# Kernel tuning notes

Measured on AMD Instinct MI355X. Metric: run time of the kernel, lower is better.

The kernel has to match this reference:

```python
import jax, jax.numpy as jnp
import numpy as np
import math

L, D, H = 4, 256, 8
HD = D // H
B, SQ, SK = 2, 1024, 1024
FF = 3 * D
EPS = 1e-5


def setup_inputs() -> dict:
    key = jax.random.key(0)
    ks = jax.random.split(key, 16)
    s = 0.02
    w = lambda k, shape: jax.random.normal(k, shape, jnp.float32) * s
    return {
        "pose": jax.random.normal(ks[0], (B, SQ, D), jnp.float32),
        "vel": jax.random.normal(ks[1], (B, SK, D), jnp.float32),
        "img": jax.random.normal(ks[2], (B, SK, D), jnp.float32),
        "Wq": w(ks[3], (L, D, D)), "bq": jnp.zeros((L, D), jnp.float32),
        "Wk": w(ks[4], (L, D, D)), "bk": jnp.zeros((L, D), jnp.float32),
        "Wv": w(ks[5], (L, D, D)), "bv": jnp.zeros((L, D), jnp.float32),
        "Wo": w(ks[6], (L, D, D)), "bo": jnp.zeros((L, D), jnp.float32),
        "an_g": jnp.ones((L, D), jnp.float32), "an_b": jnp.zeros((L, D), jnp.float32),
        "W1": w(ks[7], (L, D, FF)), "b1": jnp.zeros((L, FF), jnp.float32),
        "W2": w(ks[8], (L, FF, D)), "b2": jnp.zeros((L, D), jnp.float32),
        "fn_g": jnp.ones((L, D), jnp.float32), "fn_b": jnp.zeros((L, D), jnp.float32),
        "n_g": jnp.ones((L, D), jnp.float32), "n_b": jnp.zeros((L, D), jnp.float32),
    }


def entmax15(x):
    # exact alpha=1.5 entmax along the last axis (Peters & Martins 2019)
    x = x * 0.5
    x = x - jnp.max(x, axis=-1, keepdims=True)
    z = -jnp.sort(-x, axis=-1)  # descending
    k = jnp.arange(1, z.shape[-1] + 1, dtype=x.dtype)
    mean = jnp.cumsum(z, axis=-1) / k
    mean_sq = jnp.cumsum(z * z, axis=-1) / k
    ss = k * (mean_sq - mean * mean)
    delta = jnp.clip((1.0 - ss) / k, 0.0)
    tau = mean - jnp.sqrt(delta)
    support = jnp.sum(tau <= z, axis=-1, keepdims=True)  # support size >= 1
    tau_star = jnp.take_along_axis(tau, support - 1, axis=-1)
    p = jnp.clip(x - tau_star, 0.0)
    return p * p


def layer_norm(x, g, b):
    m = jnp.mean(x, axis=-1, keepdims=True)
    v = jnp.mean((x - m) ** 2, axis=-1, keepdims=True)
    return (x - m) * jax.lax.rsqrt(v + EPS) * g + b


def mish(x):
    return x * jnp.tanh(jax.nn.softplus(x))


def reference(pose, vel, img, Wq, bq, Wk, bk, Wv, bv, Wo, bo, an_g, an_b,
              W1, b1, W2, b2, fn_g, fn_b, n_g, n_b):
    def mha(q_in, kv, i):
        bs, sq, _ = q_in.shape
        sk = kv.shape[1]
        q = (q_in @ Wq[i] + bq[i]).reshape(bs, sq, H, HD)
        k = (kv @ Wk[i] + bk[i]).reshape(bs, sk, H, HD)
        v = (kv @ Wv[i] + bv[i]).reshape(bs, sk, H, HD)
        scores = jnp.einsum('bqhd,bkhd->bhqk', q, k) / math.sqrt(HD)
        attn = entmax15(scores)
        out = jnp.einsum('bhqk,bkhd->bqhd', attn, v).reshape(bs, sq, D)
        return out @ Wo[i] + bo[i]

    def cross_layer(x1, x2, i):
        y = layer_norm(mha(x1, x2, i), an_g[i], an_b[i])
        x1 = x1 + y
        y = layer_norm(x1, fn_g[i], fn_b[i])
        h = mish(y @ W1[i] + b1[i]) @ W2[i] + b2[i]
        return x1 + h

    def stack(x, kv):
        for i in range(L):  # small fixed layer loop (shared weights across both paths)
            mem = x
            x = cross_layer(x, kv, i)
            x = layer_norm(x, n_g[i], n_b[i])
            x = x + mem
        return x

    img_out = stack(pose, img)
    pose_out = stack(pose, vel)
    return (pose_out, img_out)
```

## Files before the change

### kernel.cpp

```cpp
#include <hip/hip_runtime.h>
#include <math.h>

#define NL   4
#define DIM  256
#define NH   8
#define HDIM 32
#define SQL  1024
#define SKL  1024
#define FFD  768
#define CB   4
#define ROWS (CB * SQL)

typedef __attribute__((ext_vector_type(8))) short bf16x8;
typedef __attribute__((ext_vector_type(4))) short bf16x4;
typedef __attribute__((ext_vector_type(4))) float f32x4;
typedef __attribute__((ext_vector_type(2))) float f32x2;


__device__ __forceinline__ short f2bf(float f) {
    union { float f; unsigned u; } v; v.f = f;
    unsigned u = v.u + 0x7fffu + ((v.u >> 16) & 1u);
    return (short)(u >> 16);
}

__device__ __forceinline__ float fast_mish(float x) {
    float u = __expf(fminf(x, 20.0f));
    float a = __builtin_fmaf(u, u, 2.0f * u);
    return x * a * __builtin_amdgcn_rcpf(a + 2.0f);
}

__device__ __forceinline__ f32x2 lo2(f32x4 v) { return __builtin_shufflevector(v, v, 0, 1); }
__device__ __forceinline__ f32x2 hi2(f32x4 v) { return __builtin_shufflevector(v, v, 2, 3); }


__global__ __launch_bounds__(256) void init_kernel(
        const float* __restrict__ pose, const float* __restrict__ vel,
        const float* __restrict__ img, float* __restrict__ X,
        short* __restrict__ Xb, short* __restrict__ KVb) {
    int idx = blockIdx.x * 256 + threadIdx.x;
    if (idx >= CB * SQL * DIM) return;
    int c = idx / (SQL * DIM);
    int rem = idx - c * (SQL * DIM);
    int b = c & 1;
    float pv = pose[b * SQL * DIM + rem];
    X[idx]  = pv;
    Xb[idx] = f2bf(pv);
    const float* kv = (c < 2) ? vel : img;
    KVb[idx] = f2bf(kv[b * SQL * DIM + rem]);
}


__global__ __launch_bounds__(256) void transpose_all(
        const float* __restrict__ Wq, const float* __restrict__ Wk,
        const float* __restrict__ Wv, const float* __restrict__ Wo,
        const float* __restrict__ W1, const float* __restrict__ W2,
        short* __restrict__ Wqt, short* __restrict__ Wkt,
        short* __restrict__ Wvt, short* __restrict__ Wot,
        short* __restrict__ W1t, short* __restrict__ W2t) {
    __shared__ float tile[64][65];
    int z = blockIdx.x;
    const float* src; short* dst; int K, N, tx, ty;
    if (z < 256) {
        int m = z >> 6, lyr = (z >> 4) & 3, r = z & 15;
        src = ((m == 0) ? Wq : (m == 1) ? Wk : (m == 2) ? Wv : Wo) + (size_t)lyr * DIM * DIM;
        dst = ((m == 0) ? Wqt : (m == 1) ? Wkt : (m == 2) ? Wvt : Wot) + (size_t)lyr * DIM * DIM;
        K = DIM; N = DIM; tx = r & 3; ty = r >> 2;
    } else if (z < 448) {
        int idx = z - 256, lyr = idx / 48, r = idx % 48;
        src = W1 + (size_t)lyr * DIM * FFD; dst = W1t + (size_t)lyr * DIM * FFD;
        K = DIM; N = FFD; tx = r % 12; ty = r / 12;
    } else {
        int idx = z - 448, lyr = idx / 48, r = idx % 48;
        src = W2 + (size_t)lyr * FFD * DIM; dst = W2t + (size_t)lyr * FFD * DIM;
        K = FFD; N = DIM; tx = r % 4; ty = r / 4;
    }
    int t = threadIdx.x;
    int n0 = tx * 64, k0 = ty * 64;
#pragma unroll
    for (int i = 0; i < 16; i++) {
        int idx = t + i * 256;
        int r = idx >> 6, c = idx & 63;
        tile[r][c] = src[(size_t)(k0 + r) * N + n0 + c];
    }
    __syncthreads();
#pragma unroll
    for (int i = 0; i < 16; i++) {
        int idx = t + i * 256;
        int r = idx >> 6, c = idx & 63;
        dst[(size_t)(n0 + r) * K + k0 + c] = f2bf(tile[c][r]);
    }
}


__global__ __launch_bounds__(256) void kv_gemm(
        const short* __restrict__ KVb, const short* __restrict__ Wkt,
        const short* __restrict__ Wvt, const float* __restrict__ bk,
        const float* __restrict__ bv, short* __restrict__ Kb4,
        short* __restrict__ Vt4) {
    int z = blockIdx.z, lyr = z >> 1, kv = z & 1;
    const short* Wt   = (kv ? Wvt : Wkt) + (size_t)lyr * DIM * DIM;
    const float* bias = (kv ? bv : bk) + (size_t)lyr * DIM;

    int t = threadIdx.x, l = t & 63, w = t >> 6;
    int lq = l & 15, lg = l >> 4;
    int bm = blockIdx.y * 64, bn = blockIdx.x * 64;

    const short* ap = KVb + (size_t)(bm + w * 16 + lq) * DIM + lg * 8;
    const short* wp = Wt + (size_t)(bn + lq) * DIM + lg * 8;

    f32x4 acc[4];
#pragma unroll
    for (int nt = 0; nt < 4; nt++) acc[nt] = (f32x4){0.f, 0.f, 0.f, 0.f};
#pragma unroll
    for (int k0 = 0; k0 < DIM; k0 += 32) {
        bf16x8 af = *(const bf16x8*)(ap + k0);
#pragma unroll
        for (int nt = 0; nt < 4; nt++) {
            bf16x8 bfr = *(const bf16x8*)(wp + (size_t)nt * 16 * DIM + k0);
            acc[nt] = __builtin_amdgcn_mfma_f32_16x16x32_bf16(af, bfr, acc[nt], 0, 0, 0);
        }
    }

    int ms = bm + w * 16 + lg * 4;
#pragma unroll
    for (int nt = 0; nt < 4; nt++) {
        int col = bn + nt * 16 + lq;
        float bv_ = bias[col];
        if (kv == 0) {
            short* out = Kb4 + (size_t)lyr * ROWS * DIM;
#pragma unroll
            for (int j = 0; j < 4; j++)
                out[(size_t)(ms + j) * DIM + col] = f2bf(acc[nt][j] + bv_);
        } else {
            int cc = ms >> 10, kl = ms & 1023;
            bf16x4 pk;
#pragma unroll
            for (int j = 0; j < 4; j++) pk[j] = f2bf(acc[nt][j] + bv_);
            *(bf16x4*)(Vt4 + (size_t)lyr * ROWS * DIM + ((size_t)(cc * DIM + col)) * SKL + kl) = pk;
        }
    }
}


__global__ __launch_bounds__(512) void fused_tail(
        const short* __restrict__ T1b, const short* __restrict__ Wot,
        const float* __restrict__ bo, const float* __restrict__ Xres,
        const float* __restrict__ ag, const float* __restrict__ ab,
        const float* __restrict__ fg, const float* __restrict__ fb,
        const short* __restrict__ W1t, const float* __restrict__ b1,
        const short* __restrict__ W2t, const float* __restrict__ b2,
        const float* __restrict__ g_, const float* __restrict__ b_,
        float* __restrict__ outf, short* __restrict__ outb) {
    __shared__ float gbuf[16][264];
    __shared__ __align__(16) short y_lds[16][280];
    __shared__ __align__(16) short g1[16][792];
    float (*xbuf)[264] = (float(*)[264])g1;

    int t = threadIdx.x, l = t & 63, w = t >> 6;
    int lq = l & 15, lg = l >> 4;
    int bm = blockIdx.x * 16;

    {
        const short* ap = T1b + (size_t)(bm + lq) * DIM + lg * 8;
        const short* wp = Wot + (size_t)(w * 32 + lq) * DIM + lg * 8;
        f32x4 acc[2];
        acc[0] = (f32x4){0.f, 0.f, 0.f, 0.f};
        acc[1] = (f32x4){0.f, 0.f, 0.f, 0.f};
#pragma unroll
        for (int k0 = 0; k0 < DIM; k0 += 32) {
            bf16x8 af = *(const bf16x8*)(ap + k0);
#pragma unroll
            for (int nt = 0; nt < 2; nt++) {
                bf16x8 bfr = *(const bf16x8*)(wp + (size_t)nt * 16 * DIM + k0);
                acc[nt] = __builtin_amdgcn_mfma_f32_16x16x32_bf16(af, bfr, acc[nt], 0, 0, 0);
            }
        }
#pragma unroll
        for (int nt = 0; nt < 2; nt++) {
            int col = w * 32 + nt * 16 + lq;
            float bv_ = bo[col];
#pragma unroll
            for (int j = 0; j < 4; j++) gbuf[lg * 4 + j][col] = acc[nt][j] + bv_;
        }
    }
    __syncthreads();

    {
        int g = t >> 5, u = t & 31;
        int row = bm + g;
        float s = 0.f, s2 = 0.f;
#pragma unroll
        for (int i = 0; i < 8; i++) {
            float v = gbuf[g][u + 32 * i];
            s += v; s2 += v * v;
        }
#pragma unroll
        for (int off = 1; off < 32; off <<= 1) { s += __shfl_xor(s, off); s2 += __shfl_xor(s2, off); }
        float m = s * (1.f / DIM);
        float rstd = rsqrtf(s2 * (1.f / DIM) - m * m + 1e-5f);

        float x1v[8];
        float sb = 0.f, sb2 = 0.f;
#pragma unroll
        for (int i = 0; i < 8; i++) {
            int col = u + 32 * i;
            float x1 = Xres[(size_t)row * DIM + col] + (gbuf[g][col] - m) * rstd * ag[col] + ab[col];
            x1v[i] = x1; sb += x1; sb2 += x1 * x1;
        }
#pragma unroll
        for (int off = 1; off < 32; off <<= 1) { sb += __shfl_xor(sb, off); sb2 += __shfl_xor(sb2, off); }
        float m2 = sb * (1.f / DIM);
        float rstd2 = rsqrtf(sb2 * (1.f / DIM) - m2 * m2 + 1e-5f);
#pragma unroll
        for (int i = 0; i < 8; i++) {
            int col = u + 32 * i;
            gbuf[g][col]  = x1v[i];
            y_lds[g][col] = f2bf((x1v[i] - m2) * rstd2 * fg[col] + fb[col]);
        }
    }
    __syncthreads();

    {
        const short* wp = W1t + (size_t)(w * 96 + lq) * DIM + lg * 8;
        f32x4 acc[6];
#pragma unroll
        for (int nt = 0; nt < 6; nt++) acc[nt] = (f32x4){0.f, 0.f, 0.f, 0.f};
#pragma unroll
        for (int k0 = 0; k0 < DIM; k0 += 32) {
            bf16x8 af = *(const bf16x8*)(&y_lds[lq][k0 + lg * 8]);
#pragma unroll
            for (int nt = 0; nt < 6; nt++) {
                bf16x8 bfr = *(const bf16x8*)(wp + (size_t)nt * 16 * DIM + k0);
                acc[nt] = __builtin_amdgcn_mfma_f32_16x16x32_bf16(af, bfr, acc[nt], 0, 0, 0);
            }
        }
#pragma unroll
        for (int nt = 0; nt < 6; nt++) {
            int col = w * 96 + nt * 16 + lq;
            float bv_ = b1[col];
#pragma unroll
            for (int j = 0; j < 4; j++)
                g1[lg * 4 + j][col] = f2bf(fast_mish(acc[nt][j] + bv_));
        }
    }
    __syncthreads();

    f32x4 acc2[2];
    acc2[0] = (f32x4){0.f, 0.f, 0.f, 0.f};
    acc2[1] = (f32x4){0.f, 0.f, 0.f, 0.f};
    {
        const short* wp2 = W2t + (size_t)(w * 32 + lq) * FFD + lg * 8;
#pragma unroll 6
        for (int ks = 0; ks < 24; ks++) {
            bf16x8 af = *(const bf16x8*)(&g1[lq][ks * 32 + lg * 8]);
#pragma unroll
            for (int nt = 0; nt < 2; nt++) {
                bf16x8 bfr = *(const bf16x8*)(wp2 + (size_t)nt * 16 * FFD + ks * 32);
                acc2[nt] = __builtin_amdgcn_mfma_f32_16x16x32_bf16(af, bfr, acc2[nt], 0, 0, 0);
            }
        }
    }
    __syncthreads();
#pragma unroll
    for (int nt = 0; nt < 2; nt++) {
        int col = w * 32 + nt * 16 + lq;
        float bv_ = b2[col];
#pragma unroll
        for (int j = 0; j < 4; j++)
            xbuf[lg * 4 + j][col] = acc2[nt][j] + bv_ + gbuf[lg * 4 + j][col];
    }
    __syncthreads();

    {
        int g = t >> 5, u = t & 31;
        int row = bm + g;
        float s = 0.f, s2 = 0.f;
#pragma unroll
        for (int i = 0; i < 8; i++) {
            float v = xbuf[g][u + 32 * i];
            s += v; s2 += v * v;
        }
#pragma unroll
        for (int off = 1; off < 32; off <<= 1) { s += __shfl_xor(s, off); s2 += __shfl_xor(s2, off); }
        float m = s * (1.f / DIM);
        float rstd = rsqrtf(s2 * (1.f / DIM) - m * m + 1e-5f);
#pragma unroll
        for (int i = 0; i < 8; i++) {
            int col = u + 32 * i;
            float o = Xres[(size_t)row * DIM + col] + (xbuf[g][col] - m) * rstd * g_[col] + b_[col];
            outf[(size_t)row * DIM + col] = o;
            if (outb) outb[(size_t)row * DIM + col] = f2bf(o);
        }
    }
}


__global__ __launch_bounds__(256, 4) void attn_mfma(
        const short* __restrict__ Xb, const short* __restrict__ Wqt,
        const float* __restrict__ bq, const short* __restrict__ K,
        const short* __restrict__ Vt, short* __restrict__ O, float qscale) {
    int id = blockIdx.x;
    int xcd = id & 7, rest = id >> 3;
    int hc = xcd * 4 + (rest >> 6);
    int c = hc & 3, h = hc >> 2;
    int qbase = (rest & 63) * 16;
    int t = threadIdx.x, l = t & 63, w = t >> 6;
    int lq = l & 15, lg = l >> 4;

    __shared__ __align__(16) short p_lds[4][16 * 256];
    __shared__ __align__(16) short q_lds[16][40];
    __shared__ __align__(16) f32x4 sred4[2][4][16];
    float* obuf = (float*)p_lds;

    if (w < 2) {
        const short* ap = Xb + (size_t)(c * SQL + qbase + lq) * DIM + lg * 8;
        const short* wp = Wqt + (size_t)(h * HDIM + w * 16 + lq) * DIM + lg * 8;
        f32x4 qa = {0.f, 0.f, 0.f, 0.f};
#pragma unroll
        for (int k0 = 0; k0 < DIM; k0 += 32) {
            bf16x8 af = *(const bf16x8*)(ap + k0);
            bf16x8 bfr = *(const bf16x8*)(wp + k0);
            qa = __builtin_amdgcn_mfma_f32_16x16x32_bf16(af, bfr, qa, 0, 0, 0);
        }
        float bb = bq[h * HDIM + w * 16 + lq];
#pragma unroll
        for (int j = 0; j < 4; j++)
            q_lds[lg * 4 + j][w * 16 + lq] = f2bf((qa[j] + bb) * qscale);
    }
    __syncthreads();
    bf16x8 qfrag = *(const bf16x8*)&q_lds[lq][lg * 8];

    const int kw = w * 256;
    f32x4 acc[16];
#pragma unroll
    for (int kt = 0; kt < 16; kt++) {
        bf16x8 kf = *(const bf16x8*)(K + ((size_t)(c * SKL + kw + kt * 16 + lq)) * DIM + h * HDIM + lg * 8);
        f32x4 z = {0.f, 0.f, 0.f, 0.f};
        acc[kt] = __builtin_amdgcn_mfma_f32_16x16x32_bf16(kf, qfrag, z, 0, 0, 0);
    }

    const f32x2 z2  = {0.f, 0.f};
    const f32x2 big = {1e30f, 1e30f};
    const f32x2 one = {1.f, 1.f};
    float tau;

    {
        f32x2 S1 = z2, S2 = z2;
#pragma unroll
        for (int kt = 0; kt < 16; kt++) {
            f32x2 x0 = lo2(acc[kt]), x1 = hi2(acc[kt]);
            S1 += x0; S1 += x1;
            S2 += x0 * x0; S2 += x1 * x1;
        }
        float sy = S1.x + S1.y, sy2 = S2.x + S2.y;
        sy  += __shfl_xor(sy, 16);  sy  += __shfl_xor(sy, 32);
        sy2 += __shfl_xor(sy2, 16); sy2 += __shfl_xor(sy2, 32);
        if (l < 16) sred4[0][w][l] = (f32x4){0.f, sy, sy2, 0.f};
        __syncthreads();
        f32x4 rr = sred4[0][0][lq] + sred4[0][1][lq] + sred4[0][2][lq] + sred4[0][3][lq];
        sy = rr[1]; sy2 = rr[2];
        const float N = (float)SKL;
        float disc = fmaxf(sy * sy - N * (sy2 - 1.0f), 0.f);
        tau = (sy - sqrtf(disc)) * (1.0f / N);
    }

    int r = 0;
    for (;;) {
        int b = 1 - (r & 1);
        f32x2 vt = {tau, tau};
        f32x2 S1 = z2, S2 = z2, NN = z2;
#pragma unroll
        for (int kt = 0; kt < 16; kt++) {
            f32x2 y0 = __builtin_elementwise_max(lo2(acc[kt]) - vt, z2);
            f32x2 y1 = __builtin_elementwise_max(hi2(acc[kt]) - vt, z2);
            S1 += y0; S1 += y1;
            S2 += y0 * y0; S2 += y1 * y1;
            NN += __builtin_elementwise_min(y0 * big, one);
            NN += __builtin_elementwise_min(y1 * big, one);
        }
        float sy = S1.x + S1.y, sy2 = S2.x + S2.y, nn = NN.x + NN.y;
        sy  += __shfl_xor(sy, 16);  sy  += __shfl_xor(sy, 32);
        sy2 += __shfl_xor(sy2, 16); sy2 += __shfl_xor(sy2, 32);
        nn  += __shfl_xor(nn, 16);  nn  += __shfl_xor(nn, 32);
        if (l < 16) sred4[b][w][l] = (f32x4){nn, sy, sy2, 0.f};
        __syncthreads();
        f32x4 rr = sred4[b][0][lq] + sred4[b][1][lq] + sred4[b][2][lq] + sred4[b][3][lq];
        nn = rr[0]; sy = rr[1]; sy2 = rr[2];
        float disc = fmaxf(sy * sy - nn * (sy2 - 1.0f), 0.f);
        float delta = (sy - sqrtf(disc)) / nn;
        tau += delta;
        r++;
        if (r >= 8 || __all(delta < 1e-6f)) break;
    }

    f32x4 o0 = {0.f, 0.f, 0.f, 0.f}, o1 = {0.f, 0.f, 0.f, 0.f};
    const short* vbase0 = Vt + ((size_t)(c * DIM + h * HDIM + lq)) * SKL;
    const short* vbase1 = vbase0 + (size_t)16 * SKL;
    {
        f32x2 vt = {tau, tau};
        int swz = lq << 4;
#pragma unroll
        for (int kt = 0; kt < 16; kt++) {
            f32x2 y0 = __builtin_elementwise_max(lo2(acc[kt]) - vt, z2);
            f32x2 y1 = __builtin_elementwise_max(hi2(acc[kt]) - vt, z2);
            f32x2 p0 = y0 * y0, p1 = y1 * y1;
            unsigned u01, u23;
            asm("v_cvt_pk_bf16_f32 %0, %1, %2" : "=v"(u01) : "v"(p0.x), "v"(p0.y));
            asm("v_cvt_pk_bf16_f32 %0, %1, %2" : "=v"(u23) : "v"(p1.x), "v"(p1.y));
            int byte = lq * 512 + ((kt * 32 + lg * 8) ^ swz);
            *(uint2*)((char*)p_lds[w] + byte) = make_uint2(u01, u23);
        }
#pragma unroll
        for (int k2 = 0; k2 < 8; k2++) {
            int byte = lq * 512 + ((k2 * 64 + lg * 16) ^ swz);
            bf16x8 pa = *(const bf16x8*)((const char*)p_lds[w] + byte);
            int k0 = kw + k2 * 32 + lg * 8;
            bf16x8 vb0 = *(const bf16x8*)(vbase0 + k0);
            bf16x8 vb1 = *(const bf16x8*)(vbase1 + k0);
            o0 = __builtin_amdgcn_mfma_f32_16x16x32_bf16(pa, vb0, o0, 0, 0, 0);
            o1 = __builtin_amdgcn_mfma_f32_16x16x32_bf16(pa, vb1, o1, 0, 0, 0);
        }
    }
    __syncthreads();

#pragma unroll
    for (int j = 0; j < 4; j++) {
        obuf[w * 512 + (lg * 4 + j) * 32 + lq]      = o0[j];
        obuf[w * 512 + (lg * 4 + j) * 32 + 16 + lq] = o1[j];
    }
    __syncthreads();
    {
        int e0 = t * 2;
        int q = e0 >> 5, d = e0 & 31;
        f32x2 s = *(const f32x2*)&obuf[e0];
#pragma unroll
        for (int ww = 1; ww < 4; ww++) s += *(const f32x2*)&obuf[ww * 512 + e0];
        unsigned uo;
        asm("v_cvt_pk_bf16_f32 %0, %1, %2" : "=v"(uo) : "v"(s.x), "v"(s.y));
        *(unsigned*)(O + ((size_t)(c * SQL + qbase + q)) * DIM + h * HDIM + d) = uo;
    }
}


extern "C" void kernel_launch(void* const* d_in, const int* in_sizes, int n_in,
                              void* d_out, int out_size, void* d_ws, size_t ws_size,
                              hipStream_t stream) {
    const float* pose = (const float*)d_in[0];
    const float* vel  = (const float*)d_in[1];
    const float* img  = (const float*)d_in[2];
    const float* Wq   = (const float*)d_in[3];
    const float* bq   = (const float*)d_in[4];
    const float* Wk   = (const float*)d_in[5];
    const float* bk   = (const float*)d_in[6];
    const float* Wv   = (const float*)d_in[7];
    const float* bv   = (const float*)d_in[8];
    const float* Wo   = (const float*)d_in[9];
    const float* bo   = (const float*)d_in[10];
    const float* an_g = (const float*)d_in[11];
    const float* an_b = (const float*)d_in[12];
    const float* W1   = (const float*)d_in[13];
    const float* b1   = (const float*)d_in[14];
    const float* W2   = (const float*)d_in[15];
    const float* b2   = (const float*)d_in[16];
    const float* fn_g = (const float*)d_in[17];
    const float* fn_b = (const float*)d_in[18];
    const float* n_g  = (const float*)d_in[19];
    const float* n_b  = (const float*)d_in[20];

    const size_t SZ = (size_t)ROWS * DIM;
    float* X    = (float*)d_ws;
    short* Xb   = (short*)(X + SZ);
    short* KVb  = Xb + SZ;
    short* T1b  = KVb + SZ;
    short* Kb4  = T1b + SZ;
    short* Vt4  = Kb4 + (size_t)NL * SZ;
    short* Wqt  = Vt4 + (size_t)NL * SZ;
    short* Wkt  = Wqt + (size_t)NL * DIM * DIM;
    short* Wvt  = Wkt + (size_t)NL * DIM * DIM;
    short* Wot  = Wvt + (size_t)NL * DIM * DIM;
    short* W1t  = Wot + (size_t)NL * DIM * DIM;
    short* W2t  = W1t + (size_t)NL * DIM * FFD;

    {
        int total = CB * SQL * DIM;
        init_kernel<<<(total + 255) / 256, 256, 0, stream>>>(pose, vel, img, X, Xb, KVb);
    }
    transpose_all<<<640, 256, 0, stream>>>(Wq, Wk, Wv, Wo, W1, W2,
                                           Wqt, Wkt, Wvt, Wot, W1t, W2t);
    kv_gemm<<<dim3(DIM / 64, ROWS / 64, 2 * NL), 256, 0, stream>>>(
        KVb, Wkt, Wvt, bk, bv, Kb4, Vt4);

    const float qscale = 0.08838834764831845f;

    for (int i = 0; i < NL; i++) {
        const short* Wqt_i = Wqt + (size_t)i * DIM * DIM;
        const short* Wot_i = Wot + (size_t)i * DIM * DIM;
        const short* W1t_i = W1t + (size_t)i * DIM * FFD;
        const short* W2t_i = W2t + (size_t)i * DIM * FFD;

        attn_mfma<<<2048, 256, 0, stream>>>(
            Xb, Wqt_i, bq + i * DIM, Kb4 + (size_t)i * SZ, Vt4 + (size_t)i * SZ,
            T1b, qscale);

        float* outp  = (i == NL - 1) ? (float*)d_out : X;
        short* outbp = (i == NL - 1) ? nullptr : Xb;
        fused_tail<<<ROWS / 16, 512, 0, stream>>>(
            T1b, Wot_i, bo + i * DIM, X,
            an_g + i * DIM, an_b + i * DIM, fn_g + i * DIM, fn_b + i * DIM,
            W1t_i, b1 + i * FFD, W2t_i, b2 + i * DIM,
            n_g + i * DIM, n_b + i * DIM, outp, outbp);
    }

    (void)in_sizes; (void)n_in; (void)out_size; (void)ws_size;
}
```

Before: 388.4 us.

## Use Newton tau updates in entmax and retile fused_tail to 8-row blocks

The entmax threshold loop in attn_mfma drops the per-element support count and its reduction. Each step is now a plain Newton update, delta = (sy2-1)/(2*sy), and the stop test uses the absolute value of delta. This cuts ALU work, shuffles and LDS traffic per iteration, but Newton may need more iterations than the support-based exact step within the 8-iteration cap, which risks both accuracy and time. Separately, fused_tail now runs 256-thread blocks covering 8 rows each, so each wave handles twice as many output columns. Half of every 16-row MFMA tile is wasted work, and weight reads per row double, in exchange for twice as many blocks.

```diff
diff --git a/kernel.cpp b/kernel.cpp
--- a/kernel.cpp
+++ b/kernel.cpp
@@ -142,7 +142,7 @@
 }
 
 
-__global__ __launch_bounds__(512) void fused_tail(
+__global__ __launch_bounds__(256) void fused_tail(
         const short* __restrict__ T1b, const short* __restrict__ Wot,
         const float* __restrict__ bo, const float* __restrict__ Xres,
         const float* __restrict__ ag, const float* __restrict__ ab,
@@ -151,36 +151,39 @@
         const short* __restrict__ W2t, const float* __restrict__ b2,
         const float* __restrict__ g_, const float* __restrict__ b_,
         float* __restrict__ outf, short* __restrict__ outb) {
-    __shared__ float gbuf[16][264];
-    __shared__ __align__(16) short y_lds[16][280];
-    __shared__ __align__(16) short g1[16][792];
+    __shared__ float gbuf[8][264];
+    __shared__ __align__(16) short y_lds[8][280];
+    __shared__ __align__(16) short g1[8][792];
     float (*xbuf)[264] = (float(*)[264])g1;
 
     int t = threadIdx.x, l = t & 63, w = t >> 6;
     int lq = l & 15, lg = l >> 4;
-    int bm = blockIdx.x * 16;
-
-    {
-        const short* ap = T1b + (size_t)(bm + lq) * DIM + lg * 8;
-        const short* wp = Wot + (size_t)(w * 32 + lq) * DIM + lg * 8;
-        f32x4 acc[2];
-        acc[0] = (f32x4){0.f, 0.f, 0.f, 0.f};
-        acc[1] = (f32x4){0.f, 0.f, 0.f, 0.f};
+    int bm = blockIdx.x * 8;
+    int arow = bm + (lq & 7);
+
+    {
+        const short* ap = T1b + (size_t)arow * DIM + lg * 8;
+        const short* wp = Wot + (size_t)(w * 64 + lq) * DIM + lg * 8;
+        f32x4 acc[4];
+#pragma unroll
+        for (int nt = 0; nt < 4; nt++) acc[nt] = (f32x4){0.f, 0.f, 0.f, 0.f};
 #pragma unroll
         for (int k0 = 0; k0 < DIM; k0 += 32) {
             bf16x8 af = *(const bf16x8*)(ap + k0);
 #pragma unroll
-            for (int nt = 0; nt < 2; nt++) {
+            for (int nt = 0; nt < 4; nt++) {
                 bf16x8 bfr = *(const bf16x8*)(wp + (size_t)nt * 16 * DIM + k0);
                 acc[nt] = __builtin_amdgcn_mfma_f32_16x16x32_bf16(af, bfr, acc[nt], 0, 0, 0);
             }
         }
-#pragma unroll
-        for (int nt = 0; nt < 2; nt++) {
-            int col = w * 32 + nt * 16 + lq;
-            float bv_ = bo[col];
-#pragma unroll
-            for (int j = 0; j < 4; j++) gbuf[lg * 4 + j][col] = acc[nt][j] + bv_;
+        if (lg < 2) {
+#pragma unroll
+            for (int nt = 0; nt < 4; nt++) {
+                int col = w * 64 + nt * 16 + lq;
+                float bv_ = bo[col];
+#pragma unroll
+                for (int j = 0; j < 4; j++) gbuf[lg * 4 + j][col] = acc[nt][j] + bv_;
+            }
         }
     }
     __syncthreads();
@@ -221,53 +224,57 @@
     __syncthreads();
 
     {
-        const short* wp = W1t + (size_t)(w * 96 + lq) * DIM + lg * 8;
-        f32x4 acc[6];
-#pragma unroll
-        for (int nt = 0; nt < 6; nt++) acc[nt] = (f32x4){0.f, 0.f, 0.f, 0.f};
+        const short* wp = W1t + (size_t)(w * 192 + lq) * DIM + lg * 8;
+        f32x4 acc[12];
+#pragma unroll
+        for (int nt = 0; nt < 12; nt++) acc[nt] = (f32x4){0.f, 0.f, 0.f, 0.f};
 #pragma unroll
         for (int k0 = 0; k0 < DIM; k0 += 32) {
-            bf16x8 af = *(const bf16x8*)(&y_lds[lq][k0 + lg * 8]);
-#pragma unroll
-            for (int nt = 0; nt < 6; nt++) {
+            bf16x8 af = *(const bf16x8*)(&y_lds[lq & 7][k0 + lg * 8]);
+#pragma unroll
+            for (int nt = 0; nt < 12; nt++) {
                 bf16x8 bfr = *(const bf16x8*)(wp + (size_t)nt * 16 * DIM + k0);
                 acc[nt] = __builtin_amdgcn_mfma_f32_16x16x32_bf16(af, bfr, acc[nt], 0, 0, 0);
             }
         }
-#pragma unroll
-        for (int nt = 0; nt < 6; nt++) {
-            int col = w * 96 + nt * 16 + lq;
-            float bv_ = b1[col];
-#pragma unroll
-            for (int j = 0; j < 4; j++)
-                g1[lg * 4 + j][col] = f2bf(fast_mish(acc[nt][j] + bv_));
-        }
-    }
-    __syncthreads();
-
-    f32x4 acc2[2];
-    acc2[0] = (f32x4){0.f, 0.f, 0.f, 0.f};
-    acc2[1] = (f32x4){0.f, 0.f, 0.f, 0.f};
-    {
-        const short* wp2 = W2t + (size_t)(w * 32 + lq) * FFD + lg * 8;
+        if (lg < 2) {
+#pragma unroll
+            for (int nt = 0; nt < 12; nt++) {
+                int col = w * 192 + nt * 16 + lq;
+                float bv_ = b1[col];
+#pragma unroll
+                for (int j = 0; j < 4; j++)
+                    g1[lg * 4 + j][col] = f2bf(fast_mish(acc[nt][j] + bv_));
+            }
+        }
+    }
+    __syncthreads();
+
+    f32x4 acc2[4];
+#pragma unroll
+    for (int nt = 0; nt < 4; nt++) acc2[nt] = (f32x4){0.f, 0.f, 0.f, 0.f};
+    {
+        const short* wp2 = W2t + (size_t)(w * 64 + lq) * FFD + lg * 8;
 #pragma unroll 6
         for (int ks = 0; ks < 24; ks++) {
-            bf16x8 af = *(const bf16x8*)(&g1[lq][ks * 32 + lg * 8]);
-#pragma unroll
-            for (int nt = 0; nt < 2; nt++) {
+            bf16x8 af = *(const bf16x8*)(&g1[lq & 7][ks * 32 + lg * 8]);
+#pragma unroll
+            for (int nt = 0; nt < 4; nt++) {
                 bf16x8 bfr = *(const bf16x8*)(wp2 + (size_t)nt * 16 * FFD + ks * 32);
                 acc2[nt] = __builtin_amdgcn_mfma_f32_16x16x32_bf16(af, bfr, acc2[nt], 0, 0, 0);
             }
         }
     }
     __syncthreads();
-#pragma unroll
-    for (int nt = 0; nt < 2; nt++) {
-        int col = w * 32 + nt * 16 + lq;
-        float bv_ = b2[col];
-#pragma unroll
-        for (int j = 0; j < 4; j++)
-            xbuf[lg * 4 + j][col] = acc2[nt][j] + bv_ + gbuf[lg * 4 + j][col];
+    if (lg < 2) {
+#pragma unroll
+        for (int nt = 0; nt < 4; nt++) {
+            int col = w * 64 + nt * 16 + lq;
+            float bv_ = b2[col];
+#pragma unroll
+            for (int j = 0; j < 4; j++)
+                xbuf[lg * 4 + j][col] = acc2[nt][j] + bv_ + gbuf[lg * 4 + j][col];
+        }
     }
     __syncthreads();
 
@@ -309,7 +316,7 @@
 
     __shared__ __align__(16) short p_lds[4][16 * 256];
     __shared__ __align__(16) short q_lds[16][40];
-    __shared__ __align__(16) f32x4 sred4[2][4][16];
+    __shared__ __align__(8) f32x2 sred2[2][4][16];
     float* obuf = (float*)p_lds;
 
     if (w < 2) {
@@ -339,9 +346,7 @@
         acc[kt] = __builtin_amdgcn_mfma_f32_16x16x32_bf16(kf, qfrag, z, 0, 0, 0);
     }
 
-    const f32x2 z2  = {0.f, 0.f};
-    const f32x2 big = {1e30f, 1e30f};
-    const f32x2 one = {1.f, 1.f};
+    const f32x2 z2 = {0.f, 0.f};
     float tau;
 
     {
@@ -355,10 +360,10 @@
         float sy = S1.x + S1.y, sy2 = S2.x + S2.y;
         sy  += __shfl_xor(sy, 16);  sy  += __shfl_xor(sy, 32);
         sy2 += __shfl_xor(sy2, 16); sy2 += __shfl_xor(sy2, 32);
-        if (l < 16) sred4[0][w][l] = (f32x4){0.f, sy, sy2, 0.f};
+        if (l < 16) sred2[0][w][l] = (f32x2){sy, sy2};
         __syncthreads();
-        f32x4 rr = sred4[0][0][lq] + sred4[0][1][lq] + sred4[0][2][lq] + sred4[0][3][lq];
-        sy = rr[1]; sy2 = rr[2];
+        f32x2 rr = sred2[0][0][lq] + sred2[0][1][lq] + sred2[0][2][lq] + sred2[0][3][lq];
+        sy = rr.x; sy2 = rr.y;
         const float N = (float)SKL;
         float disc = fmaxf(sy * sy - N * (sy2 - 1.0f), 0.f);
         tau = (sy - sqrtf(disc)) * (1.0f / N);
@@ -368,29 +373,25 @@
     for (;;) {
         int b = 1 - (r & 1);
         f32x2 vt = {tau, tau};
-        f32x2 S1 = z2, S2 = z2, NN = z2;
+        f32x2 S1 = z2, S2 = z2;
 #pragma unroll
         for (int kt = 0; kt < 16; kt++) {
             f32x2 y0 = __builtin_elementwise_max(lo2(acc[kt]) - vt, z2);
             f32x2 y1 = __builtin_elementwise_max(hi2(acc[kt]) - vt, z2);
             S1 += y0; S1 += y1;
             S2 += y0 * y0; S2 += y1 * y1;
-            NN += __builtin_elementwise_min(y0 * big, one);
-            NN += __builtin_elementwise_min(y1 * big, one);
-        }
-        float sy = S1.x + S1.y, sy2 = S2.x + S2.y, nn = NN.x + NN.y;
+        }
+        float sy = S1.x + S1.y, sy2 = S2.x + S2.y;
         sy  += __shfl_xor(sy, 16);  sy  += __shfl_xor(sy, 32);
         sy2 += __shfl_xor(sy2, 16); sy2 += __shfl_xor(sy2, 32);
-        nn  += __shfl_xor(nn, 16);  nn  += __shfl_xor(nn, 32);
-        if (l < 16) sred4[b][w][l] = (f32x4){nn, sy, sy2, 0.f};
+        if (l < 16) sred2[b][w][l] = (f32x2){sy, sy2};
         __syncthreads();
-        f32x4 rr = sred4[b][0][lq] + sred4[b][1][lq] + sred4[b][2][lq] + sred4[b][3][lq];
-        nn = rr[0]; sy = rr[1]; sy2 = rr[2];
-        float disc = fmaxf(sy * sy - nn * (sy2 - 1.0f), 0.f);
-        float delta = (sy - sqrtf(disc)) / nn;
+        f32x2 rr = sred2[b][0][lq] + sred2[b][1][lq] + sred2[b][2][lq] + sred2[b][3][lq];
+        sy = rr.x; sy2 = rr.y;
+        float delta = (sy2 - 1.0f) / (2.0f * sy);
         tau += delta;
         r++;
-        if (r >= 8 || __all(delta < 1e-6f)) break;
+        if (r >= 8 || __all(__builtin_fabsf(delta) < 1e-6f)) break;
     }
 
     f32x4 o0 = {0.f, 0.f, 0.f, 0.f}, o1 = {0.f, 0.f, 0.f, 0.f};
@@ -504,7 +505,7 @@
 
         float* outp  = (i == NL - 1) ? (float*)d_out : X;
         short* outbp = (i == NL - 1) ? nullptr : Xb;
-        fused_tail<<<ROWS / 16, 512, 0, stream>>>(
+        fused_tail<<<ROWS / 8, 256, 0, stream>>>(
             T1b, Wot_i, bo + i * DIM, X,
             an_g + i * DIM, an_b + i * DIM, fn_g + i * DIM, fn_b + i * DIM,
             W1t_i, b1 + i * FFD, W2t_i, b2 + i * DIM,
```

Result: slower. 475.1 us (+22.3%).
